# Kernel optimization log

Hardware: AMD Instinct MI355X
Metric: run time of the kernel (lower is better)

Reference implementation:

```python
import jax, jax.numpy as jnp
import numpy as np

N_VERTICES = 50000
N_RADIAL = 5
N_ANGULAR = 8
FEATURE_DIM = 64
AMT_TEMPLATES = 64
TEMPLATE_RADIUS = 0.03
ROTATION_DELTA = 1


def create_template_matrix(n_radial, n_angular, radius):
    # Polar grid of template vertices in cartesian coordinates: (R, A, 2)
    radii = radius * (np.arange(1, n_radial + 1) / n_radial)
    angles = 2.0 * np.pi * np.arange(n_angular) / n_angular
    x = radii[:, None] * np.cos(angles)[None, :]
    y = radii[:, None] * np.sin(angles)[None, :]
    return np.stack([x, y], axis=-1).astype(np.float32)


def define_interpolation_coefficients(template_matrix):
    # Gaussian interpolation prior (concrete instance of the abstract method),
    # normalized over all template vertices. Shape: (R, A, R, A)
    R, A, _ = template_matrix.shape
    flat = template_matrix.reshape(R * A, 2)
    d2 = ((flat[:, None, :] - flat[None, :, :]) ** 2).sum(-1)  # (RA, RA)
    sigma = TEMPLATE_RADIUS / N_RADIAL
    w = np.exp(-d2 / (2.0 * sigma ** 2))
    w = w / w.sum(axis=1, keepdims=True)
    return w.reshape(R, A, R, A).astype(np.float32)


def setup_inputs() -> dict:
    key = jax.random.key(0)
    k1, k2, k3, k4, k5, k6, k7 = jax.random.split(key, 7)
    mesh_signal = jax.random.normal(k1, (N_VERTICES, FEATURE_DIM), dtype=jnp.float32)
    # barycentric coordinates: [..., 0] = vertex index (stored as float),
    # [..., 1] = barycentric weight summing to 1 over the 3 triangle corners
    idx = jax.random.randint(k2, (N_VERTICES, N_RADIAL, N_ANGULAR, 3), 0, N_VERTICES)
    w = jax.random.uniform(k3, (N_VERTICES, N_RADIAL, N_ANGULAR, 3), dtype=jnp.float32)
    w = w / jnp.sum(w, axis=-1, keepdims=True)
    bary_coordinates = jnp.stack([idx.astype(jnp.float32), w], axis=-1)
    neighbor_weights = jax.random.normal(
        k4, (AMT_TEMPLATES, N_RADIAL, N_ANGULAR, FEATURE_DIM), dtype=jnp.float32) * 0.05
    center_weights = jax.random.normal(
        k5, (AMT_TEMPLATES, 1, FEATURE_DIM), dtype=jnp.float32) * 0.05
    bias = jax.random.normal(k6, (AMT_TEMPLATES,), dtype=jnp.float32) * 0.05
    tmpl = create_template_matrix(N_RADIAL, N_ANGULAR, TEMPLATE_RADIUS)
    interp_coeff = jnp.asarray(
        define_interpolation_coefficients(tmpl).reshape(N_RADIAL, N_ANGULAR, N_RADIAL * N_ANGULAR))
    return {
        "mesh_signal": mesh_signal,
        "bary_coordinates": bary_coordinates,
        "neighbor_weights": neighbor_weights,
        "center_weights": center_weights,
        "bias": bias,
        "interp_coeff": interp_coeff,
    }


def reference(mesh_signal, bary_coordinates, neighbor_weights, center_weights, bias, interp_coeff):
    N, R, A, _, _ = bary_coordinates.shape
    C = mesh_signal.shape[-1]
    T = neighbor_weights.shape[0]

    # ---- patch operator: barycentric gather + interpolation ----
    idx = bary_coordinates[..., 0].astype(jnp.int32)          # (N, R, A, 3)
    bw = bary_coordinates[..., 1]                              # (N, R, A, 3)
    gathered = mesh_signal[idx]                                # (N, R, A, 3, C)
    interp = jnp.sum(bw[..., None] * gathered, axis=-2)        # (N, R, A, C)

    # ---- prior: matvec with interpolation coefficients ----
    # original: (N,1,1,C,RA) matvec (R,A,RA) -> (N,R,A,C)
    ms = interp.reshape(N, R * A, C)                           # (N, RA, C)
    interp = jnp.einsum('nmc,ram->nrac', ms, interp_coeff)     # (N, R, A, C)

    # ---- center fold: einsum('si,tji->sjt') ----
    conv_center = jnp.einsum('nc,tjc->njt', mesh_signal, center_weights)  # (N, 1, T)

    # ---- neighbor fold over rotations ----
    # roll(interp, shift=r, axis=angular) . W == interp . roll(W, shift=-r, axis=angular)
    rotations = np.arange(0, A, ROTATION_DELTA)
    w_rot = jnp.stack([jnp.roll(neighbor_weights, -int(r), axis=2) for r in rotations])  # (O, T, R, A, C)
    conv_neighbor = jnp.einsum('nrac,otrac->not', interp, w_rot) + bias                  # (N, O, T)

    return jax.nn.relu(conv_center + conv_neighbor)
```

## Files before the change

### kernel.cpp

```cpp
#include <hip/hip_runtime.h>
#include <hip/hip_bf16.h>

#define N_V   50000
#define KTOT  2624
#define NOUT  512
#define NKB   41
#define BM    128
#define BN    256

typedef short v8s __attribute__((ext_vector_type(8)));
typedef float v4f __attribute__((ext_vector_type(4)));
typedef unsigned int v4u __attribute__((ext_vector_type(4)));
typedef unsigned short u16;
typedef unsigned int u32;

__device__ __forceinline__ u16 f2bf(float f) {
    u32 u = __float_as_uint(f);
    return (u16)((u + 0x7FFFu + ((u >> 16) & 1u)) >> 16);
}

__device__ __forceinline__ void gl2lds(const u16* g, u16* l) {
    __builtin_amdgcn_global_load_lds(
        (const __attribute__((address_space(1))) u32*)(uintptr_t)g,
        (__attribute__((address_space(3))) u32*)(uintptr_t)l, 16, 0, 0);
}

__device__ __forceinline__ u32 ipair(u32 pa, u32 pb, u32 pc, float w0, float w1, float w2) {
    float a0 = __uint_as_float(pa << 16), a1 = __uint_as_float(pa & 0xffff0000u);
    float b0 = __uint_as_float(pb << 16), b1 = __uint_as_float(pb & 0xffff0000u);
    float c0 = __uint_as_float(pc << 16), c1 = __uint_as_float(pc & 0xffff0000u);
    float r0 = w0 * a0 + w1 * b0 + w2 * c0;
    float r1 = w0 * a1 + w1 * b1 + w2 * c1;
    return __builtin_amdgcn_perm(__float_as_uint(r1) + 0x8000u,
                                 __float_as_uint(r0) + 0x8000u, 0x07060302u);
}

__global__ void cast_ms(const float* __restrict__ ms, u16* __restrict__ msb,
                        u16* __restrict__ Xc) {
    int i = (blockIdx.x * 256 + threadIdx.x) * 4;
    float4 v = *reinterpret_cast<const float4*>(ms + i);
    ushort4 o;
    o.x = f2bf(v.x); o.y = f2bf(v.y); o.z = f2bf(v.z); o.w = f2bf(v.w);
    *reinterpret_cast<ushort4*>(msb + i) = o;
    if (Xc) {
        int n = i >> 6, c = i & 63;
        *reinterpret_cast<ushort4*>(Xc + (size_t)n * KTOT + 2560 + c) = o;
    }
}

__global__ void build_w2(const float* __restrict__ nw, const float* __restrict__ cw,
                         const float* __restrict__ coeff, u16* __restrict__ w2) {
    int l = blockIdx.x * 256 + threadIdx.x;
    if (l >= NOUT * KTOT) return;
    int j = l / KTOT, k = l - j * KTOT;
    int o = j >> 6, t = j & 63;
    u16 v;
    if (k >= 2560) {
        v = f2bf(cw[t * 64 + (k - 2560)]);
    } else {
        int m = k >> 6, c = k & 63;
        float s = 0.f;
        #pragma unroll
        for (int ra = 0; ra < 40; ++ra) {
            int r = ra >> 3, a = ra & 7;
            s += coeff[ra * 40 + m] * nw[((t * 5 + r) * 8 + ((a + o) & 7)) * 64 + c];
        }
        v = f2bf(s);
    }
    w2[l] = v;
}

__global__ void build_x(const float* __restrict__ bary, const u16* __restrict__ msb,
                        u16* __restrict__ X) {
    u32 t = blockIdx.x * 256 + threadIdx.x;
    u32 n = t / 160u;
    u32 rem = t - n * 160u;
    u32 m = rem >> 2, j = rem & 3;
    const float* bb = bary + (size_t)n * 240 + m * 6;
    float2 p0 = *(const float2*)(bb);
    float2 p1 = *(const float2*)(bb + 2);
    float2 p2 = *(const float2*)(bb + 4);
    u32 jb = j * 32u;
    u32 o0 = ((u32)(int)p0.x) * 128u + jb;
    u32 o1 = ((u32)(int)p1.x) * 128u + jb;
    u32 o2 = ((u32)(int)p2.x) * 128u + jb;
    const char* mb = (const char*)msb;
    v4u a0 = *(const v4u*)(mb + o0), b0 = *(const v4u*)(mb + o0 + 16);
    v4u a1 = *(const v4u*)(mb + o1), b1 = *(const v4u*)(mb + o1 + 16);
    v4u a2 = *(const v4u*)(mb + o2), b2 = *(const v4u*)(mb + o2 + 16);
    v4u c0, c1;
    #pragma unroll
    for (int e = 0; e < 4; ++e) {
        c0[e] = ipair(a0[e], a1[e], a2[e], p0.y, p1.y, p2.y);
        c1[e] = ipair(b0[e], b1[e], b2[e], p0.y, p1.y, p2.y);
    }
    char* xp = (char*)X + (size_t)n * (KTOT * 2) + m * 128 + jb;
    *(v4u*)xp = c0;
    *(v4u*)(xp + 16) = c1;
}

__global__ __launch_bounds__(512, 4)
void gemm2(const u16* __restrict__ X, const u16* __restrict__ w2,
           const float* __restrict__ bias, float* __restrict__ out) {
    __shared__ u16 At[BM * 64];
    __shared__ u16 Bt[BN * 64];

    const int tid  = threadIdx.x;
    const int lane = tid & 63, wave = tid >> 6;
    const int l15  = lane & 15, q = lane >> 4;
    const int wm   = wave >> 2, wn = wave & 3;

    const int id = blockIdx.x;
    const int p  = (id & 7) + 8 * (id >> 4);
    const int by = (id >> 3) & 1;
    if (p >= 391) return;
    const int row0 = p * BM, col0 = by * BN;

    u32 aoff[2];
    #pragma unroll
    for (int h = 0; h < 2; ++h) {
        int slot = wave * 128 + h * 64 + lane;
        int arow = slot >> 3, ablk = (slot & 7) ^ (arow & 7);
        int grow = row0 + arow; if (grow > N_V - 1) grow = N_V - 1;
        aoff[h] = (u32)grow * (u32)KTOT + (u32)(ablk * 8);
    }
    u32 boff[4];
    #pragma unroll
    for (int i = 0; i < 4; ++i) {
        int slot = wave * 256 + i * 64 + lane;
        int brow = slot >> 3, bblk = (slot & 7) ^ (brow & 7);
        boff[i] = (u32)(col0 + brow) * (u32)KTOT + (u32)(bblk * 8);
    }

    const int eq = l15 & 7;
    const u32 a_rd0 = (u32)(wm * 64 + l15) * 128 + (u32)((q ^ eq) * 16);
    const u32 b_rd0 = (u32)(wn * 64 + l15) * 128 + (u32)((q ^ eq) * 16);

    v4f acc[4][4];
    #pragma unroll
    for (int mi = 0; mi < 4; ++mi)
        #pragma unroll
        for (int ni = 0; ni < 4; ++ni)
            acc[mi][ni] = (v4f){0.f, 0.f, 0.f, 0.f};

    #pragma unroll 1
    for (int kb = 0; kb < NKB; ++kb) {
        __syncthreads();
        #pragma unroll
        for (int h = 0; h < 2; ++h)
            gl2lds(X + aoff[h] + kb * 64, &At[wave * 1024 + h * 512]);
        #pragma unroll
        for (int i = 0; i < 4; ++i)
            gl2lds(w2 + boff[i] + kb * 64, &Bt[wave * 2048 + i * 512]);
        __syncthreads();

        const char* atp = (const char*)At;
        const char* btp = (const char*)Bt;
        #pragma unroll
        for (int s = 0; s < 2; ++s) {
            u32 ao = a_rd0 ^ (u32)(s * 64), bo = b_rd0 ^ (u32)(s * 64);
            v8s a_f[4], b_f[4];
            #pragma unroll
            for (int mi = 0; mi < 4; ++mi) a_f[mi] = *(const v8s*)(atp + ao + mi * 2048);
            #pragma unroll
            for (int ni = 0; ni < 4; ++ni) b_f[ni] = *(const v8s*)(btp + bo + ni * 2048);
            #pragma unroll
            for (int mi = 0; mi < 4; ++mi)
                #pragma unroll
                for (int ni = 0; ni < 4; ++ni)
                    acc[mi][ni] = __builtin_amdgcn_mfma_f32_16x16x32_bf16(
                        a_f[mi], b_f[ni], acc[mi][ni], 0, 0, 0);
        }
    }

    float bv[4];
    #pragma unroll
    for (int ni = 0; ni < 4; ++ni) bv[ni] = bias[ni * 16 + l15];
    #pragma unroll
    for (int mi = 0; mi < 4; ++mi) {
        int rbase = row0 + wm * 64 + mi * 16 + q * 4;
        #pragma unroll
        for (int ni = 0; ni < 4; ++ni) {
            int cg = col0 + wn * 64 + ni * 16 + l15;
            #pragma unroll
            for (int rg = 0; rg < 4; ++rg) {
                int rr = rbase + rg;
                if (rr < N_V) {
                    float v = acc[mi][ni][rg] + bv[ni];
                    out[(size_t)rr * NOUT + cg] = v > 0.f ? v : 0.f;
                }
            }
        }
    }
}

__global__ __launch_bounds__(512, 2)
void gemm_fused(const float* __restrict__ bary, const u16* __restrict__ msb,
                const u16* __restrict__ w2, const float* __restrict__ bias,
                float* __restrict__ out) {
    __shared__ u16 At[BM * 64];
    __shared__ u16 Bt[2 * BN * 64];

    const int tid  = threadIdx.x;
    const int lane = tid & 63, wave = tid >> 6;
    const int l15  = lane & 15, q = lane >> 4;
    const int wm   = wave >> 2, wn = wave & 3;

    const int id  = blockIdx.x;
    const int bx  = id % 391, by = id / 391;
    const int row0 = bx * BM, col0 = by * BN;

    const int ar  = tid >> 2;
    const u32 acb = (u32)(tid & 3) * 32;
    int an = row0 + ar; if (an > N_V - 1) an = N_V - 1;
    const u32* brow = (const u32*)bary + (size_t)an * 240;
    const u32 an_off = (u32)an * 128 + acb;

    const int e_a = ar & 7;
    const u32 at_w0 = (u32)ar * 128 + (u32)(((2 * (tid & 3)) ^ e_a) * 16);
    const u32 at_w1 = at_w0 ^ 16;

    const int eq = l15 & 7;
    const u32 a_rd0 = (u32)(wm * 64 + l15) * 128 + (u32)((q ^ eq) * 16);
    const u32 b_rd0 = (u32)(wn * 64 + l15) * 128 + (u32)((q ^ eq) * 16);

    const int rl = lane >> 3;
    const int bl = (lane & 7) ^ rl;

    v4f acc[4][4];
    #pragma unroll
    for (int mi = 0; mi < 4; ++mi)
        #pragma unroll
        for (int ni = 0; ni < 4; ++ni)
            acc[mi][ni] = (v4f){0.f, 0.f, 0.f, 0.f};

    v4u G0_0a, G0_0b, G0_1a, G0_1b, G0_2a, G0_2b;
    v4u G1_0a, G1_0b, G1_1a, G1_1b, G1_2a, G1_2b;
    v4u B0lo, B0hi, B1lo, B1hi;
    float w00, w01, w02, w10, w11, w12;
    v4u cv0, cv1;

#define BARY_LOAD(DLO, DHI, kc) do { \
    u32 _d0 = ((u32)((kc) * 6)) & ~3u; \
    DLO = *(const v4u*)(brow + _d0); \
    DHI = *(const v4u*)(brow + _d0 + 4); } while (0)

#define DECODE_ISSUE(PAR, BLO, BHI, Ga0, Gb0, Ga1, Gb1, Ga2, Gb2, W0, W1, W2) do { \
    u32 uf0, uw0, uf1, uw1, uf2, uw2; \
    if (PAR) { uf0 = BLO[2]; uw0 = BLO[3]; uf1 = BHI[0]; uw1 = BHI[1]; uf2 = BHI[2]; uw2 = BHI[3]; } \
    else     { uf0 = BLO[0]; uw0 = BLO[1]; uf1 = BLO[2]; uw1 = BLO[3]; uf2 = BHI[0]; uw2 = BHI[1]; } \
    u32 _o0 = ((u32)(int)__uint_as_float(uf0) << 7) + acb; \
    u32 _o1 = ((u32)(int)__uint_as_float(uf1) << 7) + acb; \
    u32 _o2 = ((u32)(int)__uint_as_float(uf2) << 7) + acb; \
    const char* _mb = (const char*)msb; \
    Ga0 = *(const v4u*)(_mb + _o0); Gb0 = *(const v4u*)(_mb + _o0 + 16); \
    Ga1 = *(const v4u*)(_mb + _o1); Gb1 = *(const v4u*)(_mb + _o1 + 16); \
    Ga2 = *(const v4u*)(_mb + _o2); Gb2 = *(const v4u*)(_mb + _o2 + 16); \
    W0 = __uint_as_float(uw0); W1 = __uint_as_float(uw1); W2 = __uint_as_float(uw2); } while (0)

#define CONVERT(Ga0, Gb0, Ga1, Gb1, Ga2, Gb2, W0, W1, W2) do { \
    _Pragma("unroll") \
    for (int _j = 0; _j < 4; ++_j) { \
        cv0[_j] = ipair(Ga0[_j], Ga1[_j], Ga2[_j], W0, W1, W2); \
        cv1[_j] = ipair(Gb0[_j], Gb1[_j], Gb2[_j], W0, W1, W2); } } while (0)

#define BLDS(KB_LD, BUF) do { \
    _Pragma("unroll") \
    for (int _ii = 0; _ii < 4; ++_ii) { \
        int _we = wave * 4 + _ii; \
        u32 _src = (u32)(col0 + _we * 8 + rl) * KTOT + (u32)(KB_LD) * 64 + (u32)(bl * 8); \
        gl2lds(w2 + _src, &Bt[(BUF) * (BN * 64) + _we * 512]); } } while (0)

#define AT_STORE() do { \
    *(v4u*)((char*)At + at_w0) = cv0; \
    *(v4u*)((char*)At + at_w1) = cv1; } while (0)

#define MFMA_STEP(BUF) do { \
    const char* _atp = (const char*)At; \
    const char* _btp = (const char*)Bt + (BUF) * (BN * 64 * 2); \
    _Pragma("unroll") \
    for (int _s = 0; _s < 2; ++_s) { \
        u32 _ao = a_rd0 ^ (u32)(_s * 64), _bo = b_rd0 ^ (u32)(_s * 64); \
        v8s _af[4], _bf[4]; \
        _Pragma("unroll") \
        for (int _mi = 0; _mi < 4; ++_mi) _af[_mi] = *(const v8s*)(_atp + _ao + _mi * 2048); \
        _Pragma("unroll") \
        for (int _ni = 0; _ni < 4; ++_ni) _bf[_ni] = *(const v8s*)(_btp + _bo + _ni * 2048); \
        _Pragma("unroll") \
        for (int _mi = 0; _mi < 4; ++_mi) \
            _Pragma("unroll") \
            for (int _ni = 0; _ni < 4; ++_ni) \
                acc[_mi][_ni] = __builtin_amdgcn_mfma_f32_16x16x32_bf16( \
                    _af[_mi], _bf[_ni], acc[_mi][_ni], 0, 0, 0); } } while (0)

#define BAR2_12() asm volatile("s_waitcnt vmcnt(12) lgkmcnt(0)\ns_barrier" ::: "memory")
#define BAR2_10() asm volatile("s_waitcnt vmcnt(10) lgkmcnt(0)\ns_barrier" ::: "memory")
#define BAR2_6()  asm volatile("s_waitcnt vmcnt(6) lgkmcnt(0)\ns_barrier"  ::: "memory")
#define BAR2_4()  asm volatile("s_waitcnt vmcnt(4) lgkmcnt(0)\ns_barrier"  ::: "memory")
#define BAR2_0()  asm volatile("s_waitcnt vmcnt(0) lgkmcnt(0)\ns_barrier"  ::: "memory")
#define BAR1()    asm volatile("s_barrier" ::: "memory")

    BARY_LOAD(B0lo, B0hi, 0);
    DECODE_ISSUE(0, B0lo, B0hi, G0_0a, G0_0b, G0_1a, G0_1b, G0_2a, G0_2b, w00, w01, w02);
    BARY_LOAD(B1lo, B1hi, 1);
    DECODE_ISSUE(1, B1lo, B1hi, G1_0a, G1_0b, G1_1a, G1_1b, G1_2a, G1_2b, w10, w11, w12);
    BARY_LOAD(B0lo, B0hi, 2);
    BLDS(0, 0);

    #pragma unroll 1
    for (int i = 0; i < 20; ++i) {
        {
            const int kb = 2 * i;
            CONVERT(G0_0a, G0_0b, G0_1a, G0_1b, G0_2a, G0_2b, w00, w01, w02);
            if (kb <= 36) BARY_LOAD(B1lo, B1hi, kb + 3);
            if (kb <= 37) {
                DECODE_ISSUE(0, B0lo, B0hi, G0_0a, G0_0b, G0_1a, G0_1b, G0_2a, G0_2b,
                             w00, w01, w02);
            } else if (kb == 38) {
                G0_0a = *(const v4u*)((const char*)msb + an_off);
                G0_0b = *(const v4u*)((const char*)msb + an_off + 16);
            }
            BAR1();
            BLDS(kb + 1, 1);
            AT_STORE();
            if (kb <= 36) BAR2_12(); else BAR2_6();
            MFMA_STEP(0);
        }
        {
            const int kb = 2 * i + 1;
            CONVERT(G1_0a, G1_0b, G1_1a, G1_1b, G1_2a, G1_2b, w10, w11, w12);
            if (kb <= 36) BARY_LOAD(B0lo, B0hi, kb + 3);
            if (kb <= 37)
                DECODE_ISSUE(1, B1lo, B1hi, G1_0a, G1_0b, G1_1a, G1_1b, G1_2a, G1_2b,
                             w10, w11, w12);
            BAR1();
            BLDS(kb + 1, 0);
            AT_STORE();
            if (kb <= 36) BAR2_12();
            else if (kb == 37) BAR2_10();
            else BAR2_4();
            MFMA_STEP(1);
        }
    }
    {
        cv0 = G0_0a; cv1 = G0_0b;
        BAR1();
        AT_STORE();
        BAR2_0();
        MFMA_STEP(0);
    }

    float bv[4];
    #pragma unroll
    for (int ni = 0; ni < 4; ++ni) bv[ni] = bias[ni * 16 + l15];
    #pragma unroll
    for (int mi = 0; mi < 4; ++mi) {
        int rbase = row0 + wm * 64 + mi * 16 + q * 4;
        #pragma unroll
        for (int ni = 0; ni < 4; ++ni) {
            int cg = col0 + wn * 64 + ni * 16 + l15;
            #pragma unroll
            for (int rg = 0; rg < 4; ++rg) {
                int rr = rbase + rg;
                if (rr < N_V) {
                    float v = acc[mi][ni][rg] + bv[ni];
                    out[(size_t)rr * NOUT + cg] = v > 0.f ? v : 0.f;
                }
            }
        }
    }
}

extern "C" void kernel_launch(void* const* d_in, const int* in_sizes, int n_in,
                              void* d_out, int out_size, void* d_ws, size_t ws_size,
                              hipStream_t stream) {
    const float* ms    = (const float*)d_in[0];
    const float* bary  = (const float*)d_in[1];
    const float* nw    = (const float*)d_in[2];
    const float* cw    = (const float*)d_in[3];
    const float* bias  = (const float*)d_in[4];
    const float* coeff = (const float*)d_in[5];
    float* out = (float*)d_out;

    u16* msb = (u16*)d_ws;
    u16* w2  = (u16*)((char*)d_ws + 6400000);
    const size_t x_off  = 9087104;
    const size_t x_need = x_off + (size_t)N_V * KTOT * 2;
    u16* X = (u16*)((char*)d_ws + x_off);

    if (ws_size >= x_need) {
        cast_ms<<<3125, 256, 0, stream>>>(ms, msb, X);
        build_w2<<<(NOUT * KTOT + 255) / 256, 256, 0, stream>>>(nw, cw, coeff, w2);
        build_x<<<31250, 256, 0, stream>>>(bary, msb, X);
        gemm2<<<784, 512, 0, stream>>>(X, w2, bias, out);
    } else {
        cast_ms<<<3125, 256, 0, stream>>>(ms, msb, (u16*)nullptr);
        build_w2<<<(NOUT * KTOT + 255) / 256, 256, 0, stream>>>(nw, cw, coeff, w2);
        gemm_fused<<<782, 512, 0, stream>>>(bary, msb, w2, bias, out);
    }
}
```

Baseline: 449.9 us.

## Double-buffer GEMM LDS tiles and merge prep kernels into one launch

The GEMM main loop now double-buffers the A and B LDS tiles. The next k-block is prefetched with global_load_lds while the current one feeds the MFMAs, and hand-written s_waitcnt and s_barrier sequences replace the two __syncthreads per iteration. LDS use doubles, so launch bounds drop from 4 to 2 blocks per SM, which may lower occupancy. Separately, the bf16 cast of the mesh signal and the weight-matrix build are merged into a single prep launch to save one kernel launch.

```diff
diff --git a/kernel.cpp b/kernel.cpp
--- a/kernel.cpp
+++ b/kernel.cpp
@@ -35,39 +35,40 @@
                                  __float_as_uint(r0) + 0x8000u, 0x07060302u);
 }
 
-__global__ void cast_ms(const float* __restrict__ ms, u16* __restrict__ msb,
-                        u16* __restrict__ Xc) {
-    int i = (blockIdx.x * 256 + threadIdx.x) * 4;
-    float4 v = *reinterpret_cast<const float4*>(ms + i);
-    ushort4 o;
-    o.x = f2bf(v.x); o.y = f2bf(v.y); o.z = f2bf(v.z); o.w = f2bf(v.w);
-    *reinterpret_cast<ushort4*>(msb + i) = o;
-    if (Xc) {
-        int n = i >> 6, c = i & 63;
-        *reinterpret_cast<ushort4*>(Xc + (size_t)n * KTOT + 2560 + c) = o;
-    }
-}
-
-__global__ void build_w2(const float* __restrict__ nw, const float* __restrict__ cw,
-                         const float* __restrict__ coeff, u16* __restrict__ w2) {
-    int l = blockIdx.x * 256 + threadIdx.x;
-    if (l >= NOUT * KTOT) return;
-    int j = l / KTOT, k = l - j * KTOT;
-    int o = j >> 6, t = j & 63;
-    u16 v;
-    if (k >= 2560) {
-        v = f2bf(cw[t * 64 + (k - 2560)]);
+__global__ void prep(const float* __restrict__ ms, u16* __restrict__ msb,
+                     u16* __restrict__ Xc,
+                     const float* __restrict__ nw, const float* __restrict__ cw,
+                     const float* __restrict__ coeff, u16* __restrict__ w2) {
+    if (blockIdx.x < 3125) {
+        int i = (blockIdx.x * 256 + threadIdx.x) * 4;
+        float4 v = *reinterpret_cast<const float4*>(ms + i);
+        ushort4 o;
+        o.x = f2bf(v.x); o.y = f2bf(v.y); o.z = f2bf(v.z); o.w = f2bf(v.w);
+        *reinterpret_cast<ushort4*>(msb + i) = o;
+        if (Xc) {
+            int n = i >> 6, c = i & 63;
+            *reinterpret_cast<ushort4*>(Xc + (size_t)n * KTOT + 2560 + c) = o;
+        }
     } else {
-        int m = k >> 6, c = k & 63;
-        float s = 0.f;
-        #pragma unroll
-        for (int ra = 0; ra < 40; ++ra) {
-            int r = ra >> 3, a = ra & 7;
-            s += coeff[ra * 40 + m] * nw[((t * 5 + r) * 8 + ((a + o) & 7)) * 64 + c];
-        }
-        v = f2bf(s);
-    }
-    w2[l] = v;
+        int l = (blockIdx.x - 3125) * 256 + threadIdx.x;
+        if (l >= NOUT * KTOT) return;
+        int j = l / KTOT, k = l - j * KTOT;
+        int o = j >> 6, t = j & 63;
+        u16 v;
+        if (k >= 2560) {
+            v = f2bf(cw[t * 64 + (k - 2560)]);
+        } else {
+            int m = k >> 6, c = k & 63;
+            float s = 0.f;
+            #pragma unroll
+            for (int ra = 0; ra < 40; ++ra) {
+                int r = ra >> 3, a = ra & 7;
+                s += coeff[ra * 40 + m] * nw[((t * 5 + r) * 8 + ((a + o) & 7)) * 64 + c];
+            }
+            v = f2bf(s);
+        }
+        w2[l] = v;
+    }
 }
 
 __global__ void build_x(const float* __restrict__ bary, const u16* __restrict__ msb,
@@ -99,11 +100,11 @@
     *(v4u*)(xp + 16) = c1;
 }
 
-__global__ __launch_bounds__(512, 4)
+__global__ __launch_bounds__(512, 2)
 void gemm2(const u16* __restrict__ X, const u16* __restrict__ w2,
            const float* __restrict__ bias, float* __restrict__ out) {
-    __shared__ u16 At[BM * 64];
-    __shared__ u16 Bt[BN * 64];
+    __shared__ u16 At[2 * BM * 64];
+    __shared__ u16 Bt[2 * BN * 64];
 
     const int tid  = threadIdx.x;
     const int lane = tid & 63, wave = tid >> 6;
@@ -143,19 +144,35 @@
         for (int ni = 0; ni < 4; ++ni)
             acc[mi][ni] = (v4f){0.f, 0.f, 0.f, 0.f};
 
+    #pragma unroll
+    for (int h = 0; h < 2; ++h)
+        gl2lds(X + aoff[h], &At[wave * 1024 + h * 512]);
+    #pragma unroll
+    for (int i = 0; i < 4; ++i)
+        gl2lds(w2 + boff[i], &Bt[wave * 2048 + i * 512]);
+
     #pragma unroll 1
     for (int kb = 0; kb < NKB; ++kb) {
-        __syncthreads();
-        #pragma unroll
-        for (int h = 0; h < 2; ++h)
-            gl2lds(X + aoff[h] + kb * 64, &At[wave * 1024 + h * 512]);
-        #pragma unroll
-        for (int i = 0; i < 4; ++i)
-            gl2lds(w2 + boff[i] + kb * 64, &Bt[wave * 2048 + i * 512]);
-        __syncthreads();
-
-        const char* atp = (const char*)At;
-        const char* btp = (const char*)Bt;
+        const int buf = kb & 1;
+        asm volatile("s_barrier" ::: "memory");
+
+        if (kb < NKB - 1) {
+            const int nb = buf ^ 1;
+            #pragma unroll
+            for (int h = 0; h < 2; ++h)
+                gl2lds(X + aoff[h] + (kb + 1) * 64,
+                       &At[nb * (BM * 64) + wave * 1024 + h * 512]);
+            #pragma unroll
+            for (int i = 0; i < 4; ++i)
+                gl2lds(w2 + boff[i] + (kb + 1) * 64,
+                       &Bt[nb * (BN * 64) + wave * 2048 + i * 512]);
+            asm volatile("s_waitcnt vmcnt(6)\ns_barrier" ::: "memory");
+        } else {
+            asm volatile("s_waitcnt vmcnt(0)\ns_barrier" ::: "memory");
+        }
+
+        const char* atp = (const char*)At + buf * (BM * 64 * 2);
+        const char* btp = (const char*)Bt + buf * (BN * 64 * 2);
         #pragma unroll
         for (int s = 0; s < 2; ++s) {
             u32 ao = a_rd0 ^ (u32)(s * 64), bo = b_rd0 ^ (u32)(s * 64);
@@ -388,14 +405,14 @@
     const size_t x_need = x_off + (size_t)N_V * KTOT * 2;
     u16* X = (u16*)((char*)d_ws + x_off);
 
+    const int w2_blocks = (NOUT * KTOT + 255) / 256;
+
     if (ws_size >= x_need) {
-        cast_ms<<<3125, 256, 0, stream>>>(ms, msb, X);
-        build_w2<<<(NOUT * KTOT + 255) / 256, 256, 0, stream>>>(nw, cw, coeff, w2);
+        prep<<<3125 + w2_blocks, 256, 0, stream>>>(ms, msb, X, nw, cw, coeff, w2);
         build_x<<<31250, 256, 0, stream>>>(bary, msb, X);
         gemm2<<<784, 512, 0, stream>>>(X, w2, bias, out);
     } else {
-        cast_ms<<<3125, 256, 0, stream>>>(ms, msb, (u16*)nullptr);
-        build_w2<<<(NOUT * KTOT + 255) / 256, 256, 0, stream>>>(nw, cw, coeff, w2);
+        prep<<<3125 + w2_blocks, 256, 0, stream>>>(ms, msb, (u16*)nullptr, nw, cw, coeff, w2);
         gemm_fused<<<782, 512, 0, stream>>>(bary, msb, w2, bias, out);
     }
 }
```

After: 499.7 us. 1.11x slower.
